# Optimization experiments

Measured on AMD Instinct MI355X. Metric: run time of the kernel, lower is better.

## Reference

```python
import jax, jax.numpy as jnp
import numpy as np

EPS = 1e-12  # torch F.normalize default eps


def conv1x1(x, w, b):
    # x: [N,C,H,W], w: [K,C], b: [K]
    return jnp.einsum('nchw,kc->nkhw', x, w) + b[None, :, None, None]


def forward_sa(f1, f2, cw1, cb1, cw2, cb2):
    n, _, h, w = f1.shape
    c1 = conv1x1(f1, cw1, cb1)  # [N,1,H,W]
    c2 = conv1x1(f2, cw2, cb2)
    c1 = jax.nn.softmax(c1.reshape(n, h * w), axis=1).reshape(n, 1, h, w)
    c2 = jax.nn.softmax(c2.reshape(n, h * w), axis=1).reshape(n, 1, h, w)
    return c1 * f1, c2 * f2


def l2norm_ch(x):
    # torch F.normalize(x) -> p=2 over dim=1 with eps clamp
    n = jnp.sqrt(jnp.sum(x * x, axis=1, keepdims=True))
    return x / jnp.maximum(n, EPS)


def forward_ca(f1, f2, pw1, pb1, pw2, pb2):
    N, C, H, W = f1.shape
    f1_cl = conv1x1(f1, pw1, pb1).reshape(N, -1, H * W)  # [N,Cl,HW]
    f2_cl = conv1x1(f2, pw2, pb2).reshape(N, -1, H * W)
    # A[n,p,q] = sum_c f2_cl[n,c,p] * f1_cl[n,c,q]  -> [N,HW,HW]
    A_c = jnp.tanh(jnp.einsum('ncp,ncq->npq', f2_cl, f1_cl))
    f1_v = f1.reshape(N, C, H * W)
    f2_v = f2.reshape(N, C, H * W)
    # f1_hat = f1_v @ A_c^T ; f2_hat = f2_v @ A_c
    f1_hat = jnp.einsum('ncp,nqp->ncq', f1_v, A_c).reshape(N, C, H, W)
    f2_hat = jnp.einsum('ncp,npq->ncq', f2_v, A_c).reshape(N, C, H, W)
    return l2norm_ch(f1_hat), l2norm_ch(f2_hat)


def setup_inputs() -> dict:
    key = jax.random.key(0)
    ks = jax.random.split(key, 10)
    N, C, H, W = 2, 256, 64, 64
    Cl = C // 16
    sc = 1.0 / np.sqrt(C)
    return {
        'f1': jax.random.normal(ks[0], (N, C, H, W), jnp.float32),
        'f2': jax.random.normal(ks[1], (N, C, H, W), jnp.float32),
        'pw1': jax.random.normal(ks[2], (Cl, C), jnp.float32) * sc,
        'pb1': jax.random.normal(ks[3], (Cl,), jnp.float32) * sc,
        'pw2': jax.random.normal(ks[4], (Cl, C), jnp.float32) * sc,
        'pb2': jax.random.normal(ks[5], (Cl,), jnp.float32) * sc,
        'cw1': jax.random.normal(ks[6], (1, C), jnp.float32) * sc,
        'cb1': jax.random.normal(ks[7], (1,), jnp.float32) * sc,
        'cw2': jax.random.normal(ks[8], (1, C), jnp.float32) * sc,
        'cb2': jax.random.normal(ks[9], (1,), jnp.float32) * sc,
    }


def reference(f1, f2, pw1, pb1, pw2, pb2, cw1, cb1, cw2, cb2):
    f1_1, f2_1 = forward_sa(f1, f2, cw1, cb1, cw2, cb2)
    f1_hat, f2_hat = forward_ca(f1_1, f2_1, pw1, pb1, pw2, pb2)
    fp1_hat = jax.nn.relu(f1_hat + f1)
    fp2_hat = jax.nn.relu(f2_hat + f2)
    f1_2, f2_2 = forward_sa(fp1_hat, fp2_hat, cw1, cb1, cw2, cb2)
    # Original calls forward_ca(f1_2, f2_2) again but discards the result
    # and returns (f1_2, f2_2); the dead call is omitted (identical output).
    return (f1_2, f2_2)
```

## Files before the change

kernel.cpp:

```cpp
#include <hip/hip_runtime.h>
#include <hip/hip_bf16.h>
#include <math.h>

#define N_B 2
#define C_CH 256
#define HW_SZ 4096
#define CL_CH 16

typedef __bf16 bf16x8 __attribute__((ext_vector_type(8)));
typedef float f32x4 __attribute__((ext_vector_type(4)));
typedef float f32x16 __attribute__((ext_vector_type(16)));

__device__ __forceinline__ unsigned short f2bf(float x){
  __hip_bfloat16 b = __float2bfloat16(x);
  return *reinterpret_cast<unsigned short*>(&b);
}
__device__ __forceinline__ float bf2f(unsigned short u){
  unsigned int w = ((unsigned int)u) << 16;
  return *reinterpret_cast<float*>(&w);
}
__device__ __forceinline__ unsigned int cvtpk(float a, float b){
  unsigned int r;
  asm("v_cvt_pk_bf16_f32 %0, %1, %2" : "=v"(r) : "v"(a), "v"(b));
  return r;
}
__device__ __forceinline__ float tanh_fast(float x){
  float e = __expf(2.0f * x);
  return fmaf(-2.0f, __builtin_amdgcn_rcpf(1.0f + e), 1.0f);
}
__device__ __forceinline__ void gload16(const void* gsrc, void* lds_dst){
  __builtin_amdgcn_global_load_lds(
      (const __attribute__((address_space(1))) unsigned int*)gsrc,
      (__attribute__((address_space(3))) unsigned int*)lds_dst, 16, 0, 0);
}

__global__ void k_conv1(const float* __restrict__ f1, const float* __restrict__ f2,
                        const float* __restrict__ w1, const float* __restrict__ w2,
                        const float* __restrict__ b1, const float* __restrict__ b2,
                        float* __restrict__ cv){
  const int i = blockIdx.z, n = blockIdx.y, t = threadIdx.x;
  const int ql = t & 63, cg = t >> 6;
  const int q = blockIdx.x * 64 + ql;
  const float* f = (i ? f2 : f1) + n * C_CH * HW_SZ;
  const float* w = i ? w2 : w1;
  __shared__ float ws[C_CH];
  __shared__ float red[4][72];
  ws[t] = w[t];
  __syncthreads();
  float acc = 0.f;
  #pragma unroll 8
  for (int c = cg * 64; c < cg * 64 + 64; ++c)
    acc += f[c * HW_SZ + q] * ws[c];
  red[cg][ql] = acc;
  __syncthreads();
  if (t < 64){
    float s = red[0][t] + red[1][t] + red[2][t] + red[3][t] + (i ? b2[0] : b1[0]);
    cv[(i * 2 + n) * HW_SZ + blockIdx.x * 64 + t] = s;
  }
}

__global__ void k_scale_cl(const float* __restrict__ f1, const float* __restrict__ f2,
                           const float* __restrict__ cv,
                           const float* __restrict__ pw1, const float* __restrict__ pw2,
                           const float* __restrict__ pb1, const float* __restrict__ pb2,
                           unsigned short* __restrict__ fs1, unsigned short* __restrict__ fs2,
                           unsigned short* __restrict__ clT1, unsigned short* __restrict__ clT2){
  const int i = blockIdx.z, n = blockIdx.y, t = threadIdx.x;
  const int ql = t & 63, cg = t >> 6;
  const int q = blockIdx.x * 64 + ql;
  const float* f = (i ? f2 : f1) + n * C_CH * HW_SZ;
  unsigned short* fs = (i ? fs2 : fs1) + n * C_CH * HW_SZ;
  unsigned short* clT = (i ? clT2 : clT1) + n * 32 * HW_SZ;
  const float* pw = i ? pw2 : pw1;
  const float* pb = i ? pb2 : pb1;
  const float* cvrow = cv + (i * 2 + n) * HW_SZ;
  __shared__ float wls[CL_CH * C_CH];
  __shared__ float red[4][CL_CH][66];
  __shared__ float smr[256];
  #pragma unroll
  for (int j = 0; j < 16; j++) wls[j * 256 + t] = pw[j * 256 + t];
  float sv[16];
  float m = -1e30f;
  #pragma unroll
  for (int j = 0; j < 16; j++){ sv[j] = cvrow[j * 256 + t]; m = fmaxf(m, sv[j]); }
  smr[t] = m; __syncthreads();
  for (int s = 128; s > 0; s >>= 1){ if (t < s) smr[t] = fmaxf(smr[t], smr[t + s]); __syncthreads(); }
  m = smr[0]; __syncthreads();
  float sum = 0.f;
  #pragma unroll
  for (int j = 0; j < 16; j++) sum += __expf(sv[j] - m);
  smr[t] = sum; __syncthreads();
  for (int s = 128; s > 0; s >>= 1){ if (t < s) smr[t] += smr[t + s]; __syncthreads(); }
  const float p = __expf(cvrow[q] - m) * (1.0f / smr[0]);

  float acc[16];
  #pragma unroll
  for (int k = 0; k < 16; k++) acc[k] = 0.f;
  for (int c = cg * 64; c < cg * 64 + 64; ++c){
    float vv = f[c * HW_SZ + q] * p;
    fs[c * HW_SZ + q] = f2bf(vv);
    #pragma unroll
    for (int k = 0; k < 16; k++) acc[k] += wls[k * 256 + c] * vv;
  }
  #pragma unroll
  for (int k = 0; k < 16; k++) red[cg][k][ql] = acc[k];
  __syncthreads();
  #pragma unroll
  for (int j = 0; j < 4; j++){
    int e = j * 256 + t; int k = e >> 6, qq = e & 63;
    float s = red[0][k][qq] + red[1][k][qq] + red[2][k][qq] + red[3][k][qq] + pb[k];
    clT[(blockIdx.x * 64 + qq) * 32 + k] = f2bf(s);
  }
  if (t < 128){
    uint4 zv = {0u, 0u, 0u, 0u};
    int qq = t >> 1, half = t & 1;
    *reinterpret_cast<uint4*>(&clT[(blockIdx.x * 64 + qq) * 32 + 16 + half * 8]) = zv;
  }
}

__global__ __launch_bounds__(512, 2) void k_hat(
    const unsigned short* __restrict__ fs1, const unsigned short* __restrict__ fs2,
    const unsigned short* __restrict__ clT1, const unsigned short* __restrict__ clT2,
    float* __restrict__ hat1, float* __restrict__ hat2,
    float* __restrict__ pt1, float* __restrict__ pt2){
  const int t = threadIdx.x;
  const int bid = blockIdx.x;
  const int xcd = bid & 7, slot = bid >> 3;
  const int z = xcd >> 1;
  const int n = z & 1, i = z >> 1;
  const int x = slot * 2 + (xcd & 1);
  const int qt = x >> 1, ph = x & 1;
  const int q0 = qt * 128;
  const int pbase = ph * 2048;

  const unsigned short* fs = (i ? fs2 : fs1) + n * C_CH * HW_SZ;
  const unsigned short* uT = (i ? clT1 : clT2) + n * 32 * HW_SZ;
  const unsigned short* vT = (i ? clT2 : clT1) + n * 32 * HW_SZ;
  float* out = (ph ? (i ? pt2 : pt1) : (i ? hat2 : hat1)) + n * C_CH * HW_SZ;

  __shared__ __align__(16) unsigned short fsA[2][C_CH * 64];
  __shared__ __align__(16) unsigned short aT[2][128 * 64];

  const int wv = t >> 6, l = t & 63;
  const int g4 = l >> 4, lr16 = l & 15;
  const int g2 = l >> 5, lr32 = l & 31;

  const int pfw = wv & 3;
  const int qh  = wv >> 2;
  const int cblk = wv & 3, qblk = wv >> 2;

  bf16x8 ub[4];
  #pragma unroll
  for (int j = 0; j < 4; ++j)
    ub[j] = *reinterpret_cast<const bf16x8*>(&uT[(q0 + qh * 64 + j * 16 + lr16) * 32 + g4 * 8]);

  f32x16 acc00, acc01, acc10, acc11;
  #pragma unroll
  for (int r = 0; r < 16; ++r){ acc00[r] = 0.f; acc01[r] = 0.f; acc10[r] = 0.f; acc11[r] = 0.f; }
  const f32x4 zz = {0.f, 0.f, 0.f, 0.f};

  int fs_src[4];
  #pragma unroll
  for (int it = 0; it < 4; ++it){
    int d = it * 512 + t; int c = d >> 3, sl = d & 7;
    int u = sl ^ (c & 7) ^ (((c >> 3) & 1) << 2);
    fs_src[it] = c * (HW_SZ * 2) + u * 16;
  }
  const int vgo = (pfw * 16 + lr16) * 64 + g4 * 16;
  unsigned atw0;
  {
    int qd = qh * 64 + lr16;
    int sw = (pfw * 2 + (g4 >> 1)) ^ (qd & 7) ^ (((qd >> 3) & 1) << 2);
    atw0 = qd * 128 + sw * 16 + (g4 & 1) * 8;
  }
  unsigned afo[2], bqo[2];
  #pragma unroll
  for (int cf = 0; cf < 2; ++cf){
    int crow = cblk * 64 + cf * 32 + lr32;
    afo[cf] = crow * 128 + ((g2 ^ (crow & 7) ^ (((crow >> 3) & 1) << 2)) << 4);
  }
  #pragma unroll
  for (int qf = 0; qf < 2; ++qf){
    int qrow = qblk * 64 + qf * 32 + lr32;
    bqo[qf] = qrow * 128 + ((g2 ^ (qrow & 7) ^ (((qrow >> 3) & 1) << 2)) << 4);
  }

  auto stage_fs = [&](unsigned short* dstbase, const char* src){
    #pragma unroll
    for (int it = 0; it < 4; ++it)
      gload16(src + fs_src[it], dstbase + (it * 512 + wv * 64) * 8);
  };
  auto dgen = [&](uint4 vr, char* atB){
    bf16x8 av = *reinterpret_cast<bf16x8*>(&vr);
    #pragma unroll
    for (int j = 0; j < 4; ++j){
      f32x4 d = __builtin_amdgcn_mfma_f32_16x16x32_bf16(av, ub[j], zz, 0, 0, 0);
      uint2 pk;
      pk.x = cvtpk(tanh_fast(d[0]), tanh_fast(d[1]));
      pk.y = cvtpk(tanh_fast(d[2]), tanh_fast(d[3]));
      *reinterpret_cast<uint2*>(atB + atw0 + j * 2048) = pk;
    }
  };
  auto mmain = [&](const char* faB, const char* atB){
    #pragma unroll
    for (int ks = 0; ks < 4; ++ks){
      unsigned kx = (unsigned)(ks << 5);
      bf16x8 a0 = *reinterpret_cast<const bf16x8*>(faB + (afo[0] ^ kx));
      bf16x8 a1 = *reinterpret_cast<const bf16x8*>(faB + (afo[1] ^ kx));
      bf16x8 b0 = *reinterpret_cast<const bf16x8*>(atB + (bqo[0] ^ kx));
      bf16x8 b1 = *reinterpret_cast<const bf16x8*>(atB + (bqo[1] ^ kx));
      acc00 = __builtin_amdgcn_mfma_f32_32x32x16_bf16(a0, b0, acc00, 0, 0, 0);
      acc01 = __builtin_amdgcn_mfma_f32_32x32x16_bf16(a0, b1, acc01, 0, 0, 0);
      acc10 = __builtin_amdgcn_mfma_f32_32x32x16_bf16(a1, b0, acc10, 0, 0, 0);
      acc11 = __builtin_amdgcn_mfma_f32_32x32x16_bf16(a1, b1, acc11, 0, 0, 0);
    }
  };

  const char* fpp = (const char*)fs + pbase * 2;
  const char* vp  = (const char*)vT + pbase * 64 + vgo;

  stage_fs(fsA[0], fpp); fpp += 128;
  uint4 va = *reinterpret_cast<const uint4*>(vp);
  uint4 vb = *reinterpret_cast<const uint4*>(vp + 4096);
  vp += 8192;
  dgen(va, (char*)aT[0]);

  #pragma unroll 1
  for (int k2 = 0; k2 < 16; ++k2){
    {
      stage_fs(fsA[1], fpp); fpp += 128;
      va = *reinterpret_cast<const uint4*>(vp); vp += 4096;
      dgen(vb, (char*)aT[1]);
      asm volatile("s_waitcnt lgkmcnt(0)" ::: "memory");
      __builtin_amdgcn_sched_barrier(0);
      __builtin_amdgcn_s_barrier();
      __builtin_amdgcn_sched_barrier(0);
      mmain((const char*)fsA[0], (const char*)aT[0]);
      __builtin_amdgcn_sched_barrier(0);
      __builtin_amdgcn_s_barrier();
      __builtin_amdgcn_sched_barrier(0);
    }
    {
      stage_fs(fsA[0], fpp); fpp += 128;
      vb = *reinterpret_cast<const uint4*>(vp); vp += 4096;
      dgen(va, (char*)aT[0]);
      asm volatile("s_waitcnt lgkmcnt(0)" ::: "memory");
      __builtin_amdgcn_sched_barrier(0);
      __builtin_amdgcn_s_barrier();
      __builtin_amdgcn_sched_barrier(0);
      mmain((const char*)fsA[1], (const char*)aT[1]);
      __builtin_amdgcn_sched_barrier(0);
      __builtin_amdgcn_s_barrier();
      __builtin_amdgcn_sched_barrier(0);
    }
  }

  const int qcol = q0 + qblk * 64 + lr32;
  #pragma unroll
  for (int r = 0; r < 16; ++r){
    int cr = (r & 3) + 8 * (r >> 2) + 4 * g2;
    out[(cblk * 64 + cr) * HW_SZ + qcol] = acc00[r];
    out[(cblk * 64 + cr) * HW_SZ + qcol + 32] = acc01[r];
    out[(cblk * 64 + 32 + cr) * HW_SZ + qcol] = acc10[r];
    out[(cblk * 64 + 32 + cr) * HW_SZ + qcol + 32] = acc11[r];
  }
}

__global__ void k_norm(float* __restrict__ hat1, float* __restrict__ hat2,
                       const float* __restrict__ pt1, const float* __restrict__ pt2,
                       const float* __restrict__ f1, const float* __restrict__ f2,
                       const float* __restrict__ cw1, const float* __restrict__ cw2,
                       const float* __restrict__ cb1, const float* __restrict__ cb2,
                       float* __restrict__ cv2){
  const int i = blockIdx.z, n = blockIdx.y, t = threadIdx.x;
  const int ql = t & 63, cg = t >> 6;
  const int q = blockIdx.x * 64 + ql;
  float* hat = (i ? hat2 : hat1) + n * C_CH * HW_SZ;
  const float* pt = (i ? pt2 : pt1) + n * C_CH * HW_SZ;
  const float* f = (i ? f2 : f1) + n * C_CH * HW_SZ;
  __shared__ float ws[C_CH];
  __shared__ float red[4][72];
  __shared__ float invs[64];
  __shared__ unsigned short hLs[C_CH][66];
  ws[t] = (i ? cw2 : cw1)[t];
  __syncthreads();
  float s = 0.f;
  #pragma unroll 8
  for (int c = cg * 64; c < cg * 64 + 64; ++c){
    float h = hat[c * HW_SZ + q] + pt[c * HW_SZ + q];
    hLs[c][ql] = f2bf(h);
    s += h * h;
  }
  red[cg][ql] = s; __syncthreads();
  if (t < 64){
    float ss = red[0][t] + red[1][t] + red[2][t] + red[3][t];
    invs[t] = 1.0f / fmaxf(sqrtf(ss), 1e-12f);
  }
  __syncthreads();
  const float inv = invs[ql];
  float ca = 0.f;
  #pragma unroll 8
  for (int c = cg * 64; c < cg * 64 + 64; ++c){
    float vv = fmaxf(bf2f(hLs[c][ql]) * inv + f[c * HW_SZ + q], 0.0f);
    hat[c * HW_SZ + q] = vv;
    ca += ws[c] * vv;
  }
  red[cg][ql] = ca; __syncthreads();
  if (t < 64){
    float ss = red[0][t] + red[1][t] + red[2][t] + red[3][t] + (i ? cb2[0] : cb1[0]);
    cv2[(i * 2 + n) * HW_SZ + blockIdx.x * 64 + t] = ss;
  }
}

__global__ void k_final(const float* __restrict__ fp1, const float* __restrict__ fp2,
                        const float* __restrict__ cv2, float* __restrict__ outp){
  const int i = blockIdx.z, t = threadIdx.x;
  const int idx4 = (blockIdx.x * 256 + t) * 4;
  const int n = idx4 >> 20;
  const int q = idx4 & (HW_SZ - 1);
  const float* cvrow = cv2 + (i * 2 + n) * HW_SZ;
  __shared__ float red[256];
  float sv[16];
  float m = -1e30f;
  #pragma unroll
  for (int j = 0; j < 16; j++){ sv[j] = cvrow[j * 256 + t]; m = fmaxf(m, sv[j]); }
  red[t] = m; __syncthreads();
  for (int s = 128; s > 0; s >>= 1){ if (t < s) red[t] = fmaxf(red[t], red[t + s]); __syncthreads(); }
  m = red[0]; __syncthreads();
  float sum = 0.f;
  #pragma unroll
  for (int j = 0; j < 16; j++) sum += __expf(sv[j] - m);
  red[t] = sum; __syncthreads();
  for (int s = 128; s > 0; s >>= 1){ if (t < s) red[t] += red[t + s]; __syncthreads(); }
  const float invS = 1.0f / red[0];

  const float* fp = i ? fp2 : fp1;
  float4 vv = *reinterpret_cast<const float4*>(&fp[idx4]);
  float4 o;
  o.x = vv.x * (__expf(cvrow[q + 0] - m) * invS);
  o.y = vv.y * (__expf(cvrow[q + 1] - m) * invS);
  o.z = vv.z * (__expf(cvrow[q + 2] - m) * invS);
  o.w = vv.w * (__expf(cvrow[q + 3] - m) * invS);
  *reinterpret_cast<float4*>(&outp[i * (C_CH * HW_SZ * N_B) + idx4]) = o;
}

extern "C" void kernel_launch(void* const* d_in, const int* in_sizes, int n_in,
                              void* d_out, int out_size, void* d_ws, size_t ws_size,
                              hipStream_t stream){
  const float* f1  = (const float*)d_in[0];
  const float* f2  = (const float*)d_in[1];
  const float* pw1 = (const float*)d_in[2];
  const float* pb1 = (const float*)d_in[3];
  const float* pw2 = (const float*)d_in[4];
  const float* pb2 = (const float*)d_in[5];
  const float* cw1 = (const float*)d_in[6];
  const float* cb1 = (const float*)d_in[7];
  const float* cw2 = (const float*)d_in[8];
  const float* cb2 = (const float*)d_in[9];
  float* ws = (float*)d_ws;
  float* HAT1 = ws;
  float* HAT2 = ws + 2097152;
  float* PT1  = ws + 4194304;
  float* PT2  = ws + 6291456;
  unsigned short* FS1 = (unsigned short*)(ws + 8388608);
  unsigned short* FS2 = (unsigned short*)(ws + 9437184);
  unsigned short* CLT1 = (unsigned short*)(ws + 10485760);
  unsigned short* CLT2 = (unsigned short*)(ws + 10616832);
  float* CV1  = ws + 10747904;
  float* CV2  = ws + 10764288;
  float* outp = (float*)d_out;

  k_conv1   <<<dim3(64, 2, 2), 256, 0, stream>>>(f1, f2, cw1, cw2, cb1, cb2, CV1);
  k_scale_cl<<<dim3(64, 2, 2), 256, 0, stream>>>(f1, f2, CV1, pw1, pw2, pb1, pb2,
                                                 FS1, FS2, CLT1, CLT2);
  k_hat     <<<256, 512, 0, stream>>>(FS1, FS2, CLT1, CLT2, HAT1, HAT2, PT1, PT2);
  k_norm    <<<dim3(64, 2, 2), 256, 0, stream>>>(HAT1, HAT2, PT1, PT2, f1, f2,
                                                 cw1, cw2, cb1, cb2, CV2);
  k_final   <<<dim3(2048, 1, 2), 256, 0, stream>>>(HAT1, HAT2, CV2, outp);
}
```

Before: 96.69 us.

## Halve k_hat q-tile to 64 columns and double grid for occupancy

Shrinks each k_hat block's output tile from 128 to 64 q-columns, so each wave does one B fragment and two accumulators instead of four. The grid grows from 256 to 512 blocks, the launch bound asks for 4 blocks per CU, and the attention-tile LDS buffer is halved. The aim is more parallelism and occupancy across the CUs. In exchange, each block reloads the full 256-channel fs tile for half as much output, which doubles fs staging traffic and the LDS-read to MFMA ratio.

```diff
diff --git a/kernel.cpp b/kernel.cpp
--- a/kernel.cpp
+++ b/kernel.cpp
@@ -118,7 +118,7 @@
   }
 }
 
-__global__ __launch_bounds__(512, 2) void k_hat(
+__global__ __launch_bounds__(512, 4) void k_hat(
     const unsigned short* __restrict__ fs1, const unsigned short* __restrict__ fs2,
     const unsigned short* __restrict__ clT1, const unsigned short* __restrict__ clT2,
     float* __restrict__ hat1, float* __restrict__ hat2,
@@ -130,7 +130,7 @@
   const int n = z & 1, i = z >> 1;
   const int x = slot * 2 + (xcd & 1);
   const int qt = x >> 1, ph = x & 1;
-  const int q0 = qt * 128;
+  const int q0 = qt * 64;
   const int pbase = ph * 2048;
 
   const unsigned short* fs = (i ? fs2 : fs1) + n * C_CH * HW_SZ;
@@ -139,24 +139,22 @@
   float* out = (ph ? (i ? pt2 : pt1) : (i ? hat2 : hat1)) + n * C_CH * HW_SZ;
 
   __shared__ __align__(16) unsigned short fsA[2][C_CH * 64];
-  __shared__ __align__(16) unsigned short aT[2][128 * 64];
+  __shared__ __align__(16) unsigned short aT[2][64 * 64];
 
   const int wv = t >> 6, l = t & 63;
   const int g4 = l >> 4, lr16 = l & 15;
   const int g2 = l >> 5, lr32 = l & 31;
 
   const int pfw = wv & 3;
-  const int qh  = wv >> 2;
+  const int qf0 = (wv >> 2) * 2;
   const int cblk = wv & 3, qblk = wv >> 2;
 
-  bf16x8 ub[4];
-  #pragma unroll
-  for (int j = 0; j < 4; ++j)
-    ub[j] = *reinterpret_cast<const bf16x8*>(&uT[(q0 + qh * 64 + j * 16 + lr16) * 32 + g4 * 8]);
-
-  f32x16 acc00, acc01, acc10, acc11;
-  #pragma unroll
-  for (int r = 0; r < 16; ++r){ acc00[r] = 0.f; acc01[r] = 0.f; acc10[r] = 0.f; acc11[r] = 0.f; }
+  const bf16x8 ub0 = *reinterpret_cast<const bf16x8*>(&uT[(q0 + qf0 * 16 + lr16) * 32 + g4 * 8]);
+  const bf16x8 ub1 = *reinterpret_cast<const bf16x8*>(&uT[(q0 + qf0 * 16 + 16 + lr16) * 32 + g4 * 8]);
+
+  f32x16 acc0, acc1;
+  #pragma unroll
+  for (int r = 0; r < 16; ++r){ acc0[r] = 0.f; acc1[r] = 0.f; }
   const f32x4 zz = {0.f, 0.f, 0.f, 0.f};
 
   int fs_src[4];
@@ -169,20 +167,19 @@
   const int vgo = (pfw * 16 + lr16) * 64 + g4 * 16;
   unsigned atw0;
   {
-    int qd = qh * 64 + lr16;
+    int qd = qf0 * 16 + lr16;
     int sw = (pfw * 2 + (g4 >> 1)) ^ (qd & 7) ^ (((qd >> 3) & 1) << 2);
     atw0 = qd * 128 + sw * 16 + (g4 & 1) * 8;
   }
-  unsigned afo[2], bqo[2];
+  unsigned afo[2], bqo;
   #pragma unroll
   for (int cf = 0; cf < 2; ++cf){
     int crow = cblk * 64 + cf * 32 + lr32;
     afo[cf] = crow * 128 + ((g2 ^ (crow & 7) ^ (((crow >> 3) & 1) << 2)) << 4);
   }
-  #pragma unroll
-  for (int qf = 0; qf < 2; ++qf){
-    int qrow = qblk * 64 + qf * 32 + lr32;
-    bqo[qf] = qrow * 128 + ((g2 ^ (qrow & 7) ^ (((qrow >> 3) & 1) << 2)) << 4);
+  {
+    int qrow = qblk * 32 + lr32;
+    bqo = qrow * 128 + ((g2 ^ (qrow & 7) ^ (((qrow >> 3) & 1) << 2)) << 4);
   }
 
   auto stage_fs = [&](unsigned short* dstbase, const char* src){
@@ -192,27 +189,25 @@
   };
   auto dgen = [&](uint4 vr, char* atB){
     bf16x8 av = *reinterpret_cast<bf16x8*>(&vr);
-    #pragma unroll
-    for (int j = 0; j < 4; ++j){
-      f32x4 d = __builtin_amdgcn_mfma_f32_16x16x32_bf16(av, ub[j], zz, 0, 0, 0);
-      uint2 pk;
-      pk.x = cvtpk(tanh_fast(d[0]), tanh_fast(d[1]));
-      pk.y = cvtpk(tanh_fast(d[2]), tanh_fast(d[3]));
-      *reinterpret_cast<uint2*>(atB + atw0 + j * 2048) = pk;
-    }
+    f32x4 d0 = __builtin_amdgcn_mfma_f32_16x16x32_bf16(av, ub0, zz, 0, 0, 0);
+    f32x4 d1 = __builtin_amdgcn_mfma_f32_16x16x32_bf16(av, ub1, zz, 0, 0, 0);
+    uint2 pk0, pk1;
+    pk0.x = cvtpk(tanh_fast(d0[0]), tanh_fast(d0[1]));
+    pk0.y = cvtpk(tanh_fast(d0[2]), tanh_fast(d0[3]));
+    pk1.x = cvtpk(tanh_fast(d1[0]), tanh_fast(d1[1]));
+    pk1.y = cvtpk(tanh_fast(d1[2]), tanh_fast(d1[3]));
+    *reinterpret_cast<uint2*>(atB + atw0) = pk0;
+    *reinterpret_cast<uint2*>(atB + atw0 + 2048) = pk1;
   };
   auto mmain = [&](const char* faB, const char* atB){
     #pragma unroll
     for (int ks = 0; ks < 4; ++ks){
       unsigned kx = (unsigned)(ks << 5);
+      bf16x8 b0 = *reinterpret_cast<const bf16x8*>(atB + (bqo ^ kx));
       bf16x8 a0 = *reinterpret_cast<const bf16x8*>(faB + (afo[0] ^ kx));
       bf16x8 a1 = *reinterpret_cast<const bf16x8*>(faB + (afo[1] ^ kx));
-      bf16x8 b0 = *reinterpret_cast<const bf16x8*>(atB + (bqo[0] ^ kx));
-      bf16x8 b1 = *reinterpret_cast<const bf16x8*>(atB + (bqo[1] ^ kx));
-      acc00 = __builtin_amdgcn_mfma_f32_32x32x16_bf16(a0, b0, acc00, 0, 0, 0);
-      acc01 = __builtin_amdgcn_mfma_f32_32x32x16_bf16(a0, b1, acc01, 0, 0, 0);
-      acc10 = __builtin_amdgcn_mfma_f32_32x32x16_bf16(a1, b0, acc10, 0, 0, 0);
-      acc11 = __builtin_amdgcn_mfma_f32_32x32x16_bf16(a1, b1, acc11, 0, 0, 0);
+      acc0 = __builtin_amdgcn_mfma_f32_32x32x16_bf16(a0, b0, acc0, 0, 0, 0);
+      acc1 = __builtin_amdgcn_mfma_f32_32x32x16_bf16(a1, b0, acc1, 0, 0, 0);
     }
   };
 
@@ -255,14 +250,12 @@
     }
   }
 
-  const int qcol = q0 + qblk * 64 + lr32;
+  const int qcol = q0 + qblk * 32 + lr32;
   #pragma unroll
   for (int r = 0; r < 16; ++r){
     int cr = (r & 3) + 8 * (r >> 2) + 4 * g2;
-    out[(cblk * 64 + cr) * HW_SZ + qcol] = acc00[r];
-    out[(cblk * 64 + cr) * HW_SZ + qcol + 32] = acc01[r];
-    out[(cblk * 64 + 32 + cr) * HW_SZ + qcol] = acc10[r];
-    out[(cblk * 64 + 32 + cr) * HW_SZ + qcol + 32] = acc11[r];
+    out[(cblk * 64 + cr) * HW_SZ + qcol] = acc0[r];
+    out[(cblk * 64 + 32 + cr) * HW_SZ + qcol] = acc1[r];
   }
 }
 
@@ -373,7 +366,7 @@
   k_conv1   <<<dim3(64, 2, 2), 256, 0, stream>>>(f1, f2, cw1, cw2, cb1, cb2, CV1);
   k_scale_cl<<<dim3(64, 2, 2), 256, 0, stream>>>(f1, f2, CV1, pw1, pw2, pb1, pb2,
                                                  FS1, FS2, CLT1, CLT2);
-  k_hat     <<<256, 512, 0, stream>>>(FS1, FS2, CLT1, CLT2, HAT1, HAT2, PT1, PT2);
+  k_hat     <<<512, 512, 0, stream>>>(FS1, FS2, CLT1, CLT2, HAT1, HAT2, PT1, PT2);
   k_norm    <<<dim3(64, 2, 2), 256, 0, stream>>>(HAT1, HAT2, PT1, PT2, f1, f2,
                                                  cw1, cw2, cb1, cb2, CV2);
   k_final   <<<dim3(2048, 1, 2), 256, 0, stream>>>(HAT1, HAT2, CV2, outp);
```

After: 97.84 us. No clear change (+1.2%).

## Store relu intermediate as bf16, refine LDS swizzle, raise MFMA wave priority

Applied to the files above, without the earlier changes.

k_norm now writes the post-relu intermediate as bf16 into the reused FS buffers instead of overwriting fp32 HAT, and k_final reads bf16. This halves the traffic of that intermediate. The k_hat kernel adds an extra XOR bit to its LDS swizzles for the fs and aT tiles to reduce bank conflicts, and it raises wave priority around the MFMA loop. The bf16 storage lowers the precision of the final output multiplicand.

```diff
diff --git a/kernel.cpp b/kernel.cpp
--- a/kernel.cpp
+++ b/kernel.cpp
@@ -163,7 +163,7 @@
   #pragma unroll
   for (int it = 0; it < 4; ++it){
     int d = it * 512 + t; int c = d >> 3, sl = d & 7;
-    int u = sl ^ (c & 7) ^ (((c >> 3) & 1) << 2);
+    int u = sl ^ (c & 7) ^ (((c >> 3) & 1) << 2) ^ (((c >> 4) & 1) << 1);
     fs_src[it] = c * (HW_SZ * 2) + u * 16;
   }
   const int vgo = (pfw * 16 + lr16) * 64 + g4 * 16;
@@ -177,12 +177,14 @@
   #pragma unroll
   for (int cf = 0; cf < 2; ++cf){
     int crow = cblk * 64 + cf * 32 + lr32;
-    afo[cf] = crow * 128 + ((g2 ^ (crow & 7) ^ (((crow >> 3) & 1) << 2)) << 4);
+    afo[cf] = crow * 128 +
+      ((g2 ^ (crow & 7) ^ (((crow >> 3) & 1) << 2) ^ (((crow >> 4) & 1) << 1)) << 4);
   }
   #pragma unroll
   for (int qf = 0; qf < 2; ++qf){
     int qrow = qblk * 64 + qf * 32 + lr32;
-    bqo[qf] = qrow * 128 + ((g2 ^ (qrow & 7) ^ (((qrow >> 3) & 1) << 2)) << 4);
+    bqo[qf] = qrow * 128 +
+      ((g2 ^ (qrow & 7) ^ (((qrow >> 3) & 1) << 2) ^ (((qrow >> 4) & 1) << 1)) << 4);
   }
 
   auto stage_fs = [&](unsigned short* dstbase, const char* src){
@@ -198,10 +200,12 @@
       uint2 pk;
       pk.x = cvtpk(tanh_fast(d[0]), tanh_fast(d[1]));
       pk.y = cvtpk(tanh_fast(d[2]), tanh_fast(d[3]));
-      *reinterpret_cast<uint2*>(atB + atw0 + j * 2048) = pk;
+      unsigned off = (atw0 + (unsigned)(j * 2048)) ^ ((unsigned)(j & 1) << 5);
+      *reinterpret_cast<uint2*>(atB + off) = pk;
     }
   };
   auto mmain = [&](const char* faB, const char* atB){
+    __builtin_amdgcn_s_setprio(1);
     #pragma unroll
     for (int ks = 0; ks < 4; ++ks){
       unsigned kx = (unsigned)(ks << 5);
@@ -214,6 +218,7 @@
       acc10 = __builtin_amdgcn_mfma_f32_32x32x16_bf16(a1, b0, acc10, 0, 0, 0);
       acc11 = __builtin_amdgcn_mfma_f32_32x32x16_bf16(a1, b1, acc11, 0, 0, 0);
     }
+    __builtin_amdgcn_s_setprio(0);
   };
 
   const char* fpp = (const char*)fs + pbase * 2;
@@ -266,18 +271,20 @@
   }
 }
 
-__global__ void k_norm(float* __restrict__ hat1, float* __restrict__ hat2,
+__global__ void k_norm(const float* __restrict__ hat1, const float* __restrict__ hat2,
                        const float* __restrict__ pt1, const float* __restrict__ pt2,
                        const float* __restrict__ f1, const float* __restrict__ f2,
                        const float* __restrict__ cw1, const float* __restrict__ cw2,
                        const float* __restrict__ cb1, const float* __restrict__ cb2,
+                       unsigned short* __restrict__ fpb1, unsigned short* __restrict__ fpb2,
                        float* __restrict__ cv2){
   const int i = blockIdx.z, n = blockIdx.y, t = threadIdx.x;
   const int ql = t & 63, cg = t >> 6;
   const int q = blockIdx.x * 64 + ql;
-  float* hat = (i ? hat2 : hat1) + n * C_CH * HW_SZ;
+  const float* hat = (i ? hat2 : hat1) + n * C_CH * HW_SZ;
   const float* pt = (i ? pt2 : pt1) + n * C_CH * HW_SZ;
   const float* f = (i ? f2 : f1) + n * C_CH * HW_SZ;
+  unsigned short* fpb = (i ? fpb2 : fpb1) + n * C_CH * HW_SZ;
   __shared__ float ws[C_CH];
   __shared__ float red[4][72];
   __shared__ float invs[64];
@@ -302,7 +309,7 @@
   #pragma unroll 8
   for (int c = cg * 64; c < cg * 64 + 64; ++c){
     float vv = fmaxf(bf2f(hLs[c][ql]) * inv + f[c * HW_SZ + q], 0.0f);
-    hat[c * HW_SZ + q] = vv;
+    fpb[c * HW_SZ + q] = f2bf(vv);
     ca += ws[c] * vv;
   }
   red[cg][ql] = ca; __syncthreads();
@@ -312,7 +319,8 @@
   }
 }
 
-__global__ void k_final(const float* __restrict__ fp1, const float* __restrict__ fp2,
+__global__ void k_final(const unsigned short* __restrict__ fp1,
+                        const unsigned short* __restrict__ fp2,
                         const float* __restrict__ cv2, float* __restrict__ outp){
   const int i = blockIdx.z, t = threadIdx.x;
   const int idx4 = (blockIdx.x * 256 + t) * 4;
@@ -334,13 +342,13 @@
   for (int s = 128; s > 0; s >>= 1){ if (t < s) red[t] += red[t + s]; __syncthreads(); }
   const float invS = 1.0f / red[0];
 
-  const float* fp = i ? fp2 : fp1;
-  float4 vv = *reinterpret_cast<const float4*>(&fp[idx4]);
+  const unsigned short* fp = i ? fp2 : fp1;
+  ushort4 vv = *reinterpret_cast<const ushort4*>(&fp[idx4]);
   float4 o;
-  o.x = vv.x * (__expf(cvrow[q + 0] - m) * invS);
-  o.y = vv.y * (__expf(cvrow[q + 1] - m) * invS);
-  o.z = vv.z * (__expf(cvrow[q + 2] - m) * invS);
-  o.w = vv.w * (__expf(cvrow[q + 3] - m) * invS);
+  o.x = bf2f(vv.x) * (__expf(cvrow[q + 0] - m) * invS);
+  o.y = bf2f(vv.y) * (__expf(cvrow[q + 1] - m) * invS);
+  o.z = bf2f(vv.z) * (__expf(cvrow[q + 2] - m) * invS);
+  o.w = bf2f(vv.w) * (__expf(cvrow[q + 3] - m) * invS);
   *reinterpret_cast<float4*>(&outp[i * (C_CH * HW_SZ * N_B) + idx4]) = o;
 }
 
@@ -369,12 +377,14 @@
   float* CV1  = ws + 10747904;
   float* CV2  = ws + 10764288;
   float* outp = (float*)d_out;
+  unsigned short* FPB1 = FS1;
+  unsigned short* FPB2 = FS2;
 
   k_conv1   <<<dim3(64, 2, 2), 256, 0, stream>>>(f1, f2, cw1, cw2, cb1, cb2, CV1);
   k_scale_cl<<<dim3(64, 2, 2), 256, 0, stream>>>(f1, f2, CV1, pw1, pw2, pb1, pb2,
                                                  FS1, FS2, CLT1, CLT2);
   k_hat     <<<256, 512, 0, stream>>>(FS1, FS2, CLT1, CLT2, HAT1, HAT2, PT1, PT2);
   k_norm    <<<dim3(64, 2, 2), 256, 0, stream>>>(HAT1, HAT2, PT1, PT2, f1, f2,
-                                                 cw1, cw2, cb1, cb2, CV2);
-  k_final   <<<dim3(2048, 1, 2), 256, 0, stream>>>(HAT1, HAT2, CV2, outp);
-}
+                                                 cw1, cw2, cb1, cb2, FPB1, FPB2, CV2);
+  k_final   <<<dim3(2048, 1, 2), 256, 0, stream>>>(FPB1, FPB2, CV2, outp);
+}
```

Result: no change. 97.26 us (+0.6%).

## Split main loop into two interleaved phases with prefetched LDS reads and setprio

Applied to the files above, without the earlier changes.

Restructures the fused attention/matmul loop so each k-step is split into two halves. LDS fragment loads for the MFMA block are issued before the staging and tanh-generation work, and that work is split between the halves. MFMA bursts are wrapped in s_setprio to favour the matrix pipe, and the LDS swizzle gains an extra XOR bit to reduce bank conflicts on stores and reads. This adds more barriers per iteration, plus register pressure from holding 8 fragments, in exchange for better overlap of memory, transcendental and matrix work.

```diff
diff --git a/kernel.cpp b/kernel.cpp
--- a/kernel.cpp
+++ b/kernel.cpp
@@ -163,7 +163,7 @@
   #pragma unroll
   for (int it = 0; it < 4; ++it){
     int d = it * 512 + t; int c = d >> 3, sl = d & 7;
-    int u = sl ^ (c & 7) ^ (((c >> 3) & 1) << 2);
+    int u = sl ^ (c & 7) ^ (((c >> 3) & 1) << 2) ^ (((c >> 4) & 1) << 1);
     fs_src[it] = c * (HW_SZ * 2) + u * 16;
   }
   const int vgo = (pfw * 16 + lr16) * 64 + g4 * 16;
@@ -177,82 +177,114 @@
   #pragma unroll
   for (int cf = 0; cf < 2; ++cf){
     int crow = cblk * 64 + cf * 32 + lr32;
-    afo[cf] = crow * 128 + ((g2 ^ (crow & 7) ^ (((crow >> 3) & 1) << 2)) << 4);
+    afo[cf] = crow * 128 +
+      ((g2 ^ (crow & 7) ^ (((crow >> 3) & 1) << 2) ^ (((crow >> 4) & 1) << 1)) << 4);
   }
   #pragma unroll
   for (int qf = 0; qf < 2; ++qf){
     int qrow = qblk * 64 + qf * 32 + lr32;
-    bqo[qf] = qrow * 128 + ((g2 ^ (qrow & 7) ^ (((qrow >> 3) & 1) << 2)) << 4);
-  }
-
-  auto stage_fs = [&](unsigned short* dstbase, const char* src){
+    bqo[qf] = qrow * 128 +
+      ((g2 ^ (qrow & 7) ^ (((qrow >> 3) & 1) << 2) ^ (((qrow >> 4) & 1) << 1)) << 4);
+  }
+
+  auto stage_fs = [&](char* dstbase, const char* src){
     #pragma unroll
     for (int it = 0; it < 4; ++it)
-      gload16(src + fs_src[it], dstbase + (it * 512 + wv * 64) * 8);
+      gload16(src + fs_src[it], dstbase + (it * 512 + wv * 64) * 16);
   };
-  auto dgen = [&](uint4 vr, char* atB){
+  auto dgen2 = [&](uint4 vr, char* atB, int j0){
     bf16x8 av = *reinterpret_cast<bf16x8*>(&vr);
     #pragma unroll
-    for (int j = 0; j < 4; ++j){
-      f32x4 d = __builtin_amdgcn_mfma_f32_16x16x32_bf16(av, ub[j], zz, 0, 0, 0);
+    for (int j = 0; j < 2; ++j){
+      int jj = j0 + j;
+      f32x4 d = __builtin_amdgcn_mfma_f32_16x16x32_bf16(av, ub[jj], zz, 0, 0, 0);
       uint2 pk;
       pk.x = cvtpk(tanh_fast(d[0]), tanh_fast(d[1]));
       pk.y = cvtpk(tanh_fast(d[2]), tanh_fast(d[3]));
-      *reinterpret_cast<uint2*>(atB + atw0 + j * 2048) = pk;
+      unsigned off = (atw0 + (unsigned)(jj * 2048)) ^ ((unsigned)(jj & 1) << 5);
+      *reinterpret_cast<uint2*>(atB + off) = pk;
     }
   };
-  auto mmain = [&](const char* faB, const char* atB){
-    #pragma unroll
-    for (int ks = 0; ks < 4; ++ks){
-      unsigned kx = (unsigned)(ks << 5);
-      bf16x8 a0 = *reinterpret_cast<const bf16x8*>(faB + (afo[0] ^ kx));
-      bf16x8 a1 = *reinterpret_cast<const bf16x8*>(faB + (afo[1] ^ kx));
-      bf16x8 b0 = *reinterpret_cast<const bf16x8*>(atB + (bqo[0] ^ kx));
-      bf16x8 b1 = *reinterpret_cast<const bf16x8*>(atB + (bqo[1] ^ kx));
-      acc00 = __builtin_amdgcn_mfma_f32_32x32x16_bf16(a0, b0, acc00, 0, 0, 0);
-      acc01 = __builtin_amdgcn_mfma_f32_32x32x16_bf16(a0, b1, acc01, 0, 0, 0);
-      acc10 = __builtin_amdgcn_mfma_f32_32x32x16_bf16(a1, b0, acc10, 0, 0, 0);
-      acc11 = __builtin_amdgcn_mfma_f32_32x32x16_bf16(a1, b1, acc11, 0, 0, 0);
-    }
-  };
 
   const char* fpp = (const char*)fs + pbase * 2;
   const char* vp  = (const char*)vT + pbase * 64 + vgo;
 
-  stage_fs(fsA[0], fpp); fpp += 128;
-  uint4 va = *reinterpret_cast<const uint4*>(vp);
-  uint4 vb = *reinterpret_cast<const uint4*>(vp + 4096);
-  vp += 8192;
-  dgen(va, (char*)aT[0]);
+  char *fRd = (char*)&fsA[0][0], *fWr = (char*)&fsA[1][0];
+  char *aRd = (char*)&aT[0][0],  *aWr = (char*)&aT[1][0];
+
+  stage_fs(fRd, fpp); fpp += 128;
+  uint4 vb;
+  {
+    uint4 va = *reinterpret_cast<const uint4*>(vp);
+    vb = *reinterpret_cast<const uint4*>(vp + 4096);
+    vp += 8192;
+    dgen2(va, aRd, 0);
+    dgen2(va, aRd, 2);
+  }
+  asm volatile("s_waitcnt lgkmcnt(0)" ::: "memory");
+  __builtin_amdgcn_sched_barrier(0);
+  __builtin_amdgcn_s_barrier();
+  __builtin_amdgcn_sched_barrier(0);
 
   #pragma unroll 1
-  for (int k2 = 0; k2 < 16; ++k2){
-    {
-      stage_fs(fsA[1], fpp); fpp += 128;
-      va = *reinterpret_cast<const uint4*>(vp); vp += 4096;
-      dgen(vb, (char*)aT[1]);
-      asm volatile("s_waitcnt lgkmcnt(0)" ::: "memory");
-      __builtin_amdgcn_sched_barrier(0);
-      __builtin_amdgcn_s_barrier();
-      __builtin_amdgcn_sched_barrier(0);
-      mmain((const char*)fsA[0], (const char*)aT[0]);
-      __builtin_amdgcn_sched_barrier(0);
-      __builtin_amdgcn_s_barrier();
-      __builtin_amdgcn_sched_barrier(0);
-    }
-    {
-      stage_fs(fsA[0], fpp); fpp += 128;
-      vb = *reinterpret_cast<const uint4*>(vp); vp += 4096;
-      dgen(va, (char*)aT[0]);
-      asm volatile("s_waitcnt lgkmcnt(0)" ::: "memory");
-      __builtin_amdgcn_sched_barrier(0);
-      __builtin_amdgcn_s_barrier();
-      __builtin_amdgcn_sched_barrier(0);
-      mmain((const char*)fsA[1], (const char*)aT[1]);
-      __builtin_amdgcn_sched_barrier(0);
-      __builtin_amdgcn_s_barrier();
-      __builtin_amdgcn_sched_barrier(0);
-    }
+  for (int k = 0; k < 32; ++k){
+    bf16x8 a0A = *reinterpret_cast<const bf16x8*>(fRd + afo[0]);
+    bf16x8 a1A = *reinterpret_cast<const bf16x8*>(fRd + afo[1]);
+    bf16x8 b0A = *reinterpret_cast<const bf16x8*>(aRd + bqo[0]);
+    bf16x8 b1A = *reinterpret_cast<const bf16x8*>(aRd + bqo[1]);
+    bf16x8 a0B = *reinterpret_cast<const bf16x8*>(fRd + (afo[0] ^ 32u));
+    bf16x8 a1B = *reinterpret_cast<const bf16x8*>(fRd + (afo[1] ^ 32u));
+    bf16x8 b0B = *reinterpret_cast<const bf16x8*>(aRd + (bqo[0] ^ 32u));
+    bf16x8 b1B = *reinterpret_cast<const bf16x8*>(aRd + (bqo[1] ^ 32u));
+    stage_fs(fWr, fpp); fpp += 128;
+    dgen2(vb, aWr, 0);
+    asm volatile("s_waitcnt lgkmcnt(0)" ::: "memory");
+    __builtin_amdgcn_sched_barrier(0);
+    __builtin_amdgcn_s_barrier();
+    __builtin_amdgcn_sched_barrier(0);
+    __builtin_amdgcn_s_setprio(1);
+    acc00 = __builtin_amdgcn_mfma_f32_32x32x16_bf16(a0A, b0A, acc00, 0, 0, 0);
+    acc01 = __builtin_amdgcn_mfma_f32_32x32x16_bf16(a0A, b1A, acc01, 0, 0, 0);
+    acc10 = __builtin_amdgcn_mfma_f32_32x32x16_bf16(a1A, b0A, acc10, 0, 0, 0);
+    acc11 = __builtin_amdgcn_mfma_f32_32x32x16_bf16(a1A, b1A, acc11, 0, 0, 0);
+    acc00 = __builtin_amdgcn_mfma_f32_32x32x16_bf16(a0B, b0B, acc00, 0, 0, 0);
+    acc01 = __builtin_amdgcn_mfma_f32_32x32x16_bf16(a0B, b1B, acc01, 0, 0, 0);
+    acc10 = __builtin_amdgcn_mfma_f32_32x32x16_bf16(a1B, b0B, acc10, 0, 0, 0);
+    acc11 = __builtin_amdgcn_mfma_f32_32x32x16_bf16(a1B, b1B, acc11, 0, 0, 0);
+    __builtin_amdgcn_s_setprio(0);
+    __builtin_amdgcn_sched_barrier(0);
+    __builtin_amdgcn_s_barrier();
+    __builtin_amdgcn_sched_barrier(0);
+    a0A = *reinterpret_cast<const bf16x8*>(fRd + (afo[0] ^ 64u));
+    a1A = *reinterpret_cast<const bf16x8*>(fRd + (afo[1] ^ 64u));
+    b0A = *reinterpret_cast<const bf16x8*>(aRd + (bqo[0] ^ 64u));
+    b1A = *reinterpret_cast<const bf16x8*>(aRd + (bqo[1] ^ 64u));
+    a0B = *reinterpret_cast<const bf16x8*>(fRd + (afo[0] ^ 96u));
+    a1B = *reinterpret_cast<const bf16x8*>(fRd + (afo[1] ^ 96u));
+    b0B = *reinterpret_cast<const bf16x8*>(aRd + (bqo[0] ^ 96u));
+    b1B = *reinterpret_cast<const bf16x8*>(aRd + (bqo[1] ^ 96u));
+    dgen2(vb, aWr, 2);
+    uint4 vnew = *reinterpret_cast<const uint4*>(vp); vp += 4096;
+    asm volatile("s_waitcnt vmcnt(1) lgkmcnt(0)" ::: "memory");
+    __builtin_amdgcn_sched_barrier(0);
+    __builtin_amdgcn_s_barrier();
+    __builtin_amdgcn_sched_barrier(0);
+    __builtin_amdgcn_s_setprio(1);
+    acc00 = __builtin_amdgcn_mfma_f32_32x32x16_bf16(a0A, b0A, acc00, 0, 0, 0);
+    acc01 = __builtin_amdgcn_mfma_f32_32x32x16_bf16(a0A, b1A, acc01, 0, 0, 0);
+    acc10 = __builtin_amdgcn_mfma_f32_32x32x16_bf16(a1A, b0A, acc10, 0, 0, 0);
+    acc11 = __builtin_amdgcn_mfma_f32_32x32x16_bf16(a1A, b1A, acc11, 0, 0, 0);
+    acc00 = __builtin_amdgcn_mfma_f32_32x32x16_bf16(a0B, b0B, acc00, 0, 0, 0);
+    acc01 = __builtin_amdgcn_mfma_f32_32x32x16_bf16(a0B, b1B, acc01, 0, 0, 0);
+    acc10 = __builtin_amdgcn_mfma_f32_32x32x16_bf16(a1B, b0B, acc10, 0, 0, 0);
+    acc11 = __builtin_amdgcn_mfma_f32_32x32x16_bf16(a1B, b1B, acc11, 0, 0, 0);
+    __builtin_amdgcn_s_setprio(0);
+    __builtin_amdgcn_sched_barrier(0);
+    __builtin_amdgcn_s_barrier();
+    __builtin_amdgcn_sched_barrier(0);
+    vb = vnew;
+    char* tf = fRd; fRd = fWr; fWr = tf;
+    char* ta = aRd; aRd = aWr; aWr = ta;
   }
 
   const int qcol = q0 + qblk * 64 + lr32;
```

Measured after the change: 111.9 us. 1.16x slower.
